# Kernel tuning notes

Measured on AMD Instinct MI355X. Metric: run time of the kernel, lower is better.

Reference implementation:

```python
import jax, jax.numpy as jnp
import numpy as np

B, KOBJ, NS, NK = 32, 100, 16, 8
EMB, FEAT, HID, OUT, COMB = 1024, 2052, 1024, 3000, 512


def _pseudo_coord(bb_centre):
    # bb_centre (B,K,2) -> polar pseudo coords (B,K,K,2) = (rho, theta)
    d = bb_centre[:, :, None, :] - bb_centre[:, None, :, :]
    rho = jnp.sqrt(d[..., 0] ** 2 + d[..., 1] ** 2)
    theta = jnp.arctan2(d[..., 0], d[..., 1])
    return jnp.stack([rho, theta], axis=-1)


def _gauss_weights(pseudo, mr, mt, pr, pt):
    # pseudo (B,K,NS,2); kernel params (NK,) -> weights (B,K,NS,NK)
    rho = pseudo[..., 0:1]
    theta = pseudo[..., 1:2]
    w_rho = jnp.exp(-0.5 * (rho - mr) ** 2 / (1e-14 + pr ** 2))
    fa = jnp.abs(theta - mt)
    sa = jnp.abs(2.0 * jnp.pi - fa)
    w_th = jnp.exp(-0.5 * jnp.minimum(fa, sa) ** 2 / (1e-14 + pt ** 2))
    w = w_rho * w_th
    w = jnp.where(jnp.isnan(w), 0.0, w)
    return w / jnp.sum(w, axis=-1, keepdims=True)  # normalise over kernels


def _graph_conv(feats, pseudo, conv_w, mr, mt, pr, pt):
    # feats (B,K,NS,F), conv_w (NK,F,out_k) -> (B,K,NK*out_k)
    w = _gauss_weights(pseudo, mr, mt, pr, pt)          # (B,K,NS,NK)
    agg = jnp.einsum('bksm,bksf->bkmf', w, feats)       # per-kernel neighbour sum
    out = jnp.einsum('bkmf,mfo->bkmo', agg, conv_w)     # per-kernel linear
    return out.reshape(out.shape[0], out.shape[1], -1)  # kernel-major concat


def _neighbourhood(feats, pseudo, adj, weight):
    # topk over adjacency rows; softmax over topk values (== the per-row loop softmax)
    top_v, top_i = jax.lax.top_k(adj, NS)               # (B,K,NS)
    a = jax.nn.softmax(top_v, axis=-1)
    nb_f = jax.vmap(lambda f, i: f[i])(feats, top_i)    # (B,K,NS,F)
    nb_p = jnp.take_along_axis(pseudo, top_i[..., None], axis=2)  # (B,K,NS,2)
    if weight:
        nb_f = a[..., None] * nb_f
    return nb_f, nb_p


def _forward(question, image, K, W_lproj, b_lproj, W_e1, b_e1, W_e2, b_e2,
             conv_w1, mean_rho1, mean_theta1, prec_rho1, prec_theta1,
             conv_w2, mean_rho2, mean_theta2, prec_rho2, prec_theta2,
             W_o1, b_o1, W_o2, b_o2):
    bb = image[:, :, -4:]
    bb_size = bb[:, :, 2:] - bb[:, :, :2]
    bb_centre = bb[:, :, :2] + 0.5 * bb_size
    pseudo = _pseudo_coord(bb_centre)                   # (B,K,K,2)

    qenc = question @ W_lproj + b_lproj                 # (B,HID)
    qrep = jnp.broadcast_to(qenc[:, None, :], (image.shape[0], K, qenc.shape[-1]))
    cat = jnp.concatenate([image, qrep], axis=-1)       # (B,K,FEAT+HID)

    # GraphLearner: two relu linears then gram matrix
    h = jax.nn.relu(cat @ W_e1 + b_e1)
    h = jax.nn.relu(h @ W_e2 + b_e2)                    # (B,K,COMB)
    adj = jnp.einsum('bkc,blc->bkl', h, h)              # (B,K,K)

    nb_f, nb_p = _neighbourhood(image, pseudo, adj, weight=True)
    g1 = jax.nn.relu(_graph_conv(nb_f, nb_p, conv_w1, mean_rho1, mean_theta1, prec_rho1, prec_theta1))
    nb_f2, nb_p2 = _neighbourhood(g1, pseudo, adj, weight=False)
    g2 = jax.nn.relu(_graph_conv(nb_f2, nb_p2, conv_w2, mean_rho2, mean_theta2, prec_rho2, prec_theta2))
    g2 = jnp.max(g2, axis=1)                            # (B,HID)

    hh = jax.nn.relu(qenc) * g2
    h1 = jax.nn.relu(hh @ W_o1 + b_o1)
    logits = h1 @ W_o2 + b_o2
    return logits, adj


def setup_inputs() -> dict:
    key = jax.random.key(0)
    ks = jax.random.split(key, 17)
    s = jnp.float32(0.02)
    f32 = jnp.float32
    inp = {
        'question': jax.random.normal(ks[0], (B, EMB), f32),
        'image': jax.random.uniform(ks[1], (B, KOBJ, FEAT), f32),
        'K': KOBJ,
        'W_lproj': jax.random.normal(ks[2], (EMB, HID), f32) * s,
        'b_lproj': jnp.zeros((HID,), f32),
        'W_e1': jax.random.normal(ks[3], (FEAT + HID, COMB), f32) * s,
        'b_e1': jnp.zeros((COMB,), f32),
        'W_e2': jax.random.normal(ks[4], (COMB, COMB), f32) * s,
        'b_e2': jnp.zeros((COMB,), f32),
        'conv_w1': jax.random.normal(ks[5], (NK, FEAT, 2 * HID // NK), f32) * s,
        'mean_rho1': jax.random.uniform(ks[6], (NK,), f32),
        'mean_theta1': jax.random.uniform(ks[7], (NK,), f32, -np.pi, np.pi),
        'prec_rho1': jax.random.uniform(ks[8], (NK,), f32),
        'prec_theta1': jax.random.uniform(ks[9], (NK,), f32),
        'conv_w2': jax.random.normal(ks[10], (NK, 2 * HID, HID // NK), f32) * s,
        'mean_rho2': jax.random.uniform(ks[11], (NK,), f32),
        'mean_theta2': jax.random.uniform(ks[12], (NK,), f32, -np.pi, np.pi),
        'prec_rho2': jax.random.uniform(ks[13], (NK,), f32),
        'prec_theta2': jax.random.uniform(ks[14], (NK,), f32),
        'W_o1': jax.random.normal(ks[15], (HID, OUT), f32) * s,
        'b_o1': jnp.zeros((OUT,), f32),
        'W_o2': jax.random.normal(ks[16], (OUT, OUT), f32) * s,
        'b_o2': jnp.zeros((OUT,), f32),
    }
    return inp


def reference(question, image, K, W_lproj, b_lproj, W_e1, b_e1, W_e2, b_e2,
              conv_w1, mean_rho1, mean_theta1, prec_rho1, prec_theta1,
              conv_w2, mean_rho2, mean_theta2, prec_rho2, prec_theta2,
              W_o1, b_o1, W_o2, b_o2):
    return _forward(question, image, K, W_lproj, b_lproj, W_e1, b_e1, W_e2, b_e2,
                    conv_w1, mean_rho1, mean_theta1, prec_rho1, prec_theta1,
                    conv_w2, mean_rho2, mean_theta2, prec_rho2, prec_theta2,
                    W_o1, b_o1, W_o2, b_o2)
```

## Files before the change

### kernel.cpp

```cpp
#include <hip/hip_runtime.h>
#include <math.h>
#include <stdint.h>

#define B_    32
#define KOBJ  100
#define NS_   16
#define NK_   8
#define EMB_  1024
#define FEAT_ 2052
#define HID_  1024
#define OUT_  3000
#define COMB_ 512

#define KP1   2112
#define KP2   2048
#define NO_P  3072
#define KO2   3008

typedef __attribute__((ext_vector_type(8))) short s16x8;
typedef __attribute__((ext_vector_type(4))) float f32x4;

__device__ inline short f2bf(float f) {
  uint32_t u = __builtin_bit_cast(uint32_t, f);
  u = (u + 0x7fff + ((u >> 16) & 1)) >> 16;
  return (short)u;
}
__device__ inline float bf2f(short s) {
  uint32_t u = ((uint32_t)(uint16_t)s) << 16;
  return __builtin_bit_cast(float, u);
}
__device__ inline void gload_lds16(const void* g, void* l) {
  __builtin_amdgcn_global_load_lds(
      (const __attribute__((address_space(1))) void*)g,
      (__attribute__((address_space(3))) void*)l, 16, 0, 0);
}
__device__ inline int xcd_remap(int fid, int nwg) {
  int q = nwg >> 3, r = nwg & 7;
  int x = fid & 7, l = fid >> 3;
  return (x < r ? x * (q + 1) : r * (q + 1) + (x - r) * q) + l;
}

#define IMG_CHUNKS (B_ * KOBJ * (KP1 / 8))
#define IMG_BLKS   ((IMG_CHUNKS + 255) / 256)
#define Q_CHUNKS   (B_ * (EMB_ / 8))
#define Q_BLKS     ((Q_CHUNKS + 255) / 256)
#define C_BLKS     ((B_ * KOBJ + 255) / 256)

__device__ inline void cvt8_split(const float* __restrict__ in, short* __restrict__ oh,
                                  short* __restrict__ ol, int K, int Kp, int idx) {
  int row = idx / (Kp / 8), c8 = (idx % (Kp / 8)) * 8;
  float f[8];
  if (c8 + 8 <= K) {
    const float* src = in + (size_t)row * K + c8;
    float4 a = *(const float4*)src;
    float4 b = *(const float4*)(src + 4);
    f[0] = a.x; f[1] = a.y; f[2] = a.z; f[3] = a.w;
    f[4] = b.x; f[5] = b.y; f[6] = b.z; f[7] = b.w;
  } else {
#pragma unroll
    for (int i = 0; i < 8; ++i) {
      int k = c8 + i;
      f[i] = (k < K) ? in[(size_t)row * K + k] : 0.f;
    }
  }
  s16x8 vh, vl;
#pragma unroll
  for (int i = 0; i < 8; ++i) {
    short h = f2bf(f[i]);
    vh[i] = h;
    vl[i] = f2bf(f[i] - bf2f(h));
  }
  *(s16x8*)(oh + (size_t)row * Kp + c8) = vh;
  *(s16x8*)(ol + (size_t)row * Kp + c8) = vl;
}

__global__ __launch_bounds__(256) void prep_inputs(
    const float* __restrict__ image, const float* __restrict__ question,
    short* __restrict__ imgb, short* __restrict__ imgl,
    short* __restrict__ qh, short* __restrict__ ql, float* __restrict__ cent) {
  int bb = blockIdx.x, tid = threadIdx.x;
  if (bb < IMG_BLKS) {
    int idx = bb * 256 + tid;
    if (idx < IMG_CHUNKS) cvt8_split(image, imgb, imgl, FEAT_, KP1, idx);
  } else if (bb < IMG_BLKS + Q_BLKS) {
    int idx = (bb - IMG_BLKS) * 256 + tid;
    if (idx < Q_CHUNKS) cvt8_split(question, qh, ql, EMB_, EMB_, idx);
  } else {
    int i = (bb - IMG_BLKS - Q_BLKS) * 256 + tid;
    if (i < B_ * KOBJ) {
      const float* bbx = image + (size_t)i * FEAT_ + (FEAT_ - 4);
      cent[i * 2 + 0] = 0.5f * (bbx[0] + bbx[2]);
      cent[i * 2 + 1] = 0.5f * (bbx[1] + bbx[3]);
    }
  }
}

struct TD {
  const float* in; short* oh; short* ol;
  int K, N, Kp, OPM, nkt, split, conv, cum;
};
struct TDs { TD d[8]; };

__global__ __launch_bounds__(256) void transpose_all(TDs ds) {
  __shared__ float s[64][65];
  int bid = blockIdx.x;
  int i = 0;
  while (i < 7 && bid >= ds.d[i].cum) ++i;
  const TD& d = ds.d[i];
  int local = bid - (i ? ds.d[i - 1].cum : 0);
  int k0 = (local % d.nkt) * 64, n0 = (local / d.nkt) * 64;
  int t = threadIdx.x;
  int rr = t >> 4, c4 = (t & 15) * 4;
  bool fullN = d.conv || (n0 + 64 <= d.N);
#pragma unroll
  for (int p = 0; p < 4; ++p) {
    int row = p * 16 + rr;
    int kg = k0 + row;
    float v0 = 0.f, v1 = 0.f, v2 = 0.f, v3 = 0.f;
    if (kg < d.K) {
      const float* src = d.conv
          ? d.in + ((size_t)(n0 / d.OPM) * d.K + kg) * d.OPM + (n0 % d.OPM) + c4
          : d.in + (size_t)kg * d.N + n0 + c4;
      if (fullN) {
        float4 v = *(const float4*)src;
        v0 = v.x; v1 = v.y; v2 = v.z; v3 = v.w;
      } else {
        int nb = n0 + c4;
        if (nb + 0 < d.N) v0 = src[0];
        if (nb + 1 < d.N) v1 = src[1];
        if (nb + 2 < d.N) v2 = src[2];
        if (nb + 3 < d.N) v3 = src[3];
      }
    }
    s[row][c4 + 0] = v0; s[row][c4 + 1] = v1;
    s[row][c4 + 2] = v2; s[row][c4 + 3] = v3;
  }
  __syncthreads();
  int nl = t >> 2, kc = (t & 3) << 4;
#pragma unroll
  for (int half = 0; half < 2; ++half) {
    s16x8 vh, vl;
#pragma unroll
    for (int j = 0; j < 8; ++j) {
      float f = s[kc + half * 8 + j][nl];
      short h = f2bf(f);
      vh[j] = h;
      vl[j] = f2bf(f - bf2f(h));
    }
    size_t o = (size_t)(n0 + nl) * d.Kp + k0 + kc + half * 8;
    *(s16x8*)(d.oh + o) = vh;
    if (d.split) *(s16x8*)(d.ol + o) = vl;
  }
}

template <int BM, int BN, int WR, int WC, bool SPLIT, bool RELU, bool BIAS, int OMODE,
          bool SPLITK, bool PB16>
__device__ __forceinline__ void gemm_body(
    char* smem, int bx, int by, int bz,
    const short* __restrict__ Ah, const short* __restrict__ Al,
    const short* __restrict__ Bh, const short* __restrict__ Bl,
    const float* __restrict__ bias,
    float* __restrict__ Cf, short* __restrict__ Ch, short* __restrict__ Cl,
    float* __restrict__ part, short* __restrict__ partb, int KS,
    int M, int N, int Kp, int ldc, int Nw) {
  constexpr int NWV = WR * WC;
  constexpr int WM = BM / WR, WN = BN / WC;
  constexpr int FM = WM / 16, FN = WN / 16;
  constexpr int ACH = BM / 8, BCH = BN / 8;
  constexpr int NCH = (ACH + BCH) * (SPLIT ? 2 : 1);
  char* AshC = smem;
  char* BshC = smem + BM * 128;
  char* AslC = smem + (BM + BN) * 128;
  char* BslC = smem + (2 * BM + BN) * 128;
  int tid = threadIdx.x, wave = tid >> 6, lane = tid & 63;
  int wr = wave / WC, wc = wave % WC;
  int r16 = lane & 15, kq = lane >> 4;
  int m0 = by * BM, n0 = bx * BN;
  int kb = SPLITK ? bz * KS : 0;
  int ke = SPLITK ? (kb + KS < Kp ? kb + KS : Kp) : Kp;
  f32x4 acc[FM][FN] = {};

  for (int k0 = kb; k0 < ke; k0 += 64) {
    __syncthreads();
    for (int c = wave; c < NCH; c += NWV) {
      int cc = c;
      const short* g;
      char* l;
      bool isA;
      if (cc < ACH) { isA = true; g = Ah; l = AshC; }
      else if (SPLIT && cc < 2 * ACH) { cc -= ACH; isA = true; g = Al; l = AslC; }
      else {
        cc -= SPLIT ? 2 * ACH : ACH;
        if (cc < BCH) { isA = false; g = Bh; l = BshC; }
        else { cc -= BCH; isA = false; g = Bl; l = BslC; }
      }
      int Lb = cc * 1024 + lane * 16;
      int row = Lb >> 7;
      int off = (Lb & 127) ^ ((row & 7) << 4);
      const short* gsrc = g + (size_t)((isA ? m0 : n0) + row) * Kp + k0 + (off >> 1);
      gload_lds16(gsrc, l + cc * 1024);
    }
    __syncthreads();
#pragma unroll
    for (int kk = 0; kk < 2; ++kk) {
      int woff = kk * 64 + kq * 16;
      s16x8 ah[FM], al[FM], bh[FN], bl[FN];
#pragma unroll
      for (int f = 0; f < FM; ++f) {
        int row = wr * WM + f * 16 + r16;
        int o = woff ^ ((row & 7) << 4);
        ah[f] = *(const s16x8*)(AshC + row * 128 + o);
        if (SPLIT) al[f] = *(const s16x8*)(AslC + row * 128 + o);
      }
#pragma unroll
      for (int gg = 0; gg < FN; ++gg) {
        int row = wc * WN + gg * 16 + r16;
        int o = woff ^ ((row & 7) << 4);
        bh[gg] = *(const s16x8*)(BshC + row * 128 + o);
        if (SPLIT) bl[gg] = *(const s16x8*)(BslC + row * 128 + o);
      }
#pragma unroll
      for (int f = 0; f < FM; ++f)
#pragma unroll
        for (int gg = 0; gg < FN; ++gg) {
          acc[f][gg] = __builtin_amdgcn_mfma_f32_16x16x32_bf16(ah[f], bh[gg], acc[f][gg], 0, 0, 0);
          if (SPLIT) {
            acc[f][gg] = __builtin_amdgcn_mfma_f32_16x16x32_bf16(ah[f], bl[gg], acc[f][gg], 0, 0, 0);
            acc[f][gg] = __builtin_amdgcn_mfma_f32_16x16x32_bf16(al[f], bh[gg], acc[f][gg], 0, 0, 0);
          }
        }
    }
  }
#pragma unroll
  for (int f = 0; f < FM; ++f)
#pragma unroll
    for (int gg = 0; gg < FN; ++gg)
#pragma unroll
      for (int r = 0; r < 4; ++r) {
        int m = m0 + wr * WM + f * 16 + (lane >> 4) * 4 + r;
        int n = n0 + wc * WN + gg * 16 + r16;
        if (m >= M || n >= Nw) continue;
        float v = (n < N) ? acc[f][gg][r] : 0.f;
        size_t idx = (size_t)m * ldc + n;
        if (SPLITK) {
          size_t pidx = (size_t)bz * M * ldc + idx;
          if (PB16) partb[pidx] = f2bf(v);
          else      part[pidx] = v;
        } else {
          if (BIAS && n < N) v += bias[n];
          if (RELU) v = fmaxf(v, 0.f);
          if (OMODE == 0) Cf[idx] = v;
          else if (OMODE == 1) {
            short h = f2bf(v);
            Ch[idx] = h;
            Cl[idx] = f2bf(v - bf2f(h));
          } else if (OMODE == 2) {
            Ch[idx] = f2bf(v);
          } else {
            Cf[idx] = v;
            short h = f2bf(v);
            Ch[idx] = h;
            Cl[idx] = f2bf(v - bf2f(h));
          }
        }
      }
}

template <int BM, int BN, int WR, int WC, bool SPLIT, bool RELU, bool BIAS, int OMODE,
          bool SPLITK, bool PB16>
__global__ __launch_bounds__(WR * WC * 64) void gemm_mx(
    const short* __restrict__ Ah, const short* __restrict__ Al,
    const short* __restrict__ Bh, const short* __restrict__ Bl,
    const float* __restrict__ bias,
    float* __restrict__ Cf, short* __restrict__ Ch, short* __restrict__ Cl,
    float* __restrict__ part, short* __restrict__ partb, int KS,
    int M, int N, int Kp, int ldc, int Nw) {
  __shared__ char smem_s[(BM + BN) * 128 * (SPLIT ? 2 : 1)];
  int gx = gridDim.x, gy = gridDim.y, gz = gridDim.z;
  int fid = (blockIdx.z * gy + blockIdx.y) * gx + blockIdx.x;
  int wg = xcd_remap(fid, gx * gy * gz);
  int bx = wg % gx, byz = wg / gx;
  int by = byz % gy, bz = byz / gy;
  gemm_body<BM, BN, WR, WC, SPLIT, RELU, BIAS, OMODE, SPLITK, PB16>(
      smem_s, bx, by, bz, Ah, Al, Bh, Bl, bias, Cf, Ch, Cl, part, partb, KS,
      M, N, Kp, ldc, Nw);
}

#define E1B 800
#define P1B 800
__global__ __launch_bounds__(512) void fused_e1_proj1(
    const short* __restrict__ imgb, const short* __restrict__ imgl,
    const short* __restrict__ we1ah, const short* __restrict__ we1al,
    float* __restrict__ partE,
    const short* __restrict__ cw1t, short* __restrict__ partP) {
  extern __shared__ char smem[];
  int fid = blockIdx.x;
  if (fid < E1B) {
    int wg = xcd_remap(fid, E1B);
    int gx = COMB_ / 64;
    int bx = wg % gx, t = wg / gx;
    int by = t % (B_ * KOBJ / 128), bz = t / (B_ * KOBJ / 128);
    gemm_body<128, 64, 4, 2, true, false, false, 0, true, false>(
        smem, bx, by, bz, imgb, imgl, we1ah, we1al, nullptr,
        nullptr, nullptr, nullptr, partE, nullptr, 576,
        B_ * KOBJ, COMB_, KP1, COMB_, COMB_);
  } else {
    int wg = xcd_remap(fid - E1B, P1B);
    int gx = 2 * HID_ / 128;
    int bx = wg % gx, t = wg / gx;
    int by = t % (B_ * KOBJ / 128), bz = t / (B_ * KOBJ / 128);
    gemm_body<128, 128, 2, 4, false, false, false, 0, true, true>(
        smem, bx, by, bz, imgb, nullptr, cw1t, nullptr, nullptr,
        nullptr, nullptr, nullptr, nullptr, partP, 1056,
        B_ * KOBJ, 2 * HID_, KP1, 2 * HID_, 2 * HID_);
  }
}

template <int OMODE, bool RELU, bool BIAS, bool BCAST, bool PB16>
__global__ void reduce_split(const float* __restrict__ part, const short* __restrict__ partb,
                             int SK, size_t pstride,
                             const float* __restrict__ bias, const float* __restrict__ bcast,
                             int bcols, float* __restrict__ Cf, short* __restrict__ Ch,
                             short* __restrict__ Cl, int M, int N, int ldIn, int ldOut) {
  int idx4 = blockIdx.x * 256 + threadIdx.x;
  int ld4 = ldIn >> 2;
  if (idx4 >= M * ld4) return;
  int m = idx4 / ld4;
  int n = (idx4 - m * ld4) << 2;
  size_t base = (size_t)m * ldIn + n;
  float a[4] = {0.f, 0.f, 0.f, 0.f};
  for (int s = 0; s < SK; ++s) {
    if (PB16) {
      short4 p = *(const short4*)(partb + (size_t)s * pstride + base);
      const short* pp = (const short*)&p;
#pragma unroll
      for (int j = 0; j < 4; ++j) a[j] += bf2f(pp[j]);
    } else {
      float4 p = *(const float4*)(part + (size_t)s * pstride + base);
      a[0] += p.x; a[1] += p.y; a[2] += p.z; a[3] += p.w;
    }
  }
#pragma unroll
  for (int j = 0; j < 4; ++j) {
    int nn = n + j;
    if (nn < N) {
      if (BCAST) a[j] += bcast[(size_t)(m / KOBJ) * bcols + nn];
      if (BIAS) a[j] += bias[nn];
    }
    if (RELU) a[j] = fmaxf(a[j], 0.f);
  }
  if (n >= ldOut) return;
  size_t o = (size_t)m * ldOut + n;
  if (OMODE == 0) {
    *(float4*)(Cf + o) = make_float4(a[0], a[1], a[2], a[3]);
  } else if (OMODE == 1) {
    short4 hh, ll;
    short* hp = (short*)&hh; short* lp = (short*)&ll;
#pragma unroll
    for (int j = 0; j < 4; ++j) {
      short h = f2bf(a[j]);
      hp[j] = h;
      lp[j] = f2bf(a[j] - bf2f(h));
    }
    *(short4*)(Ch + o) = hh;
    *(short4*)(Cl + o) = ll;
  } else {
    short4 hh;
    short* hp = (short*)&hh;
#pragma unroll
    for (int j = 0; j < 4; ++j) hp[j] = f2bf(a[j]);
    *(short4*)(Ch + o) = hh;
  }
}

__global__ __launch_bounds__(512) void adj_mfma(const short* __restrict__ Hh,
                                                const short* __restrict__ Hl,
                                                float* __restrict__ adj) {
  __shared__ short Ash[128 * 64];
  __shared__ short Asl[128 * 64];
  int tid = threadIdx.x, wave = tid >> 6, lane = tid & 63;
  int wr = wave >> 2, wc = wave & 3;
  int r16 = lane & 15, kq = lane >> 4;
  int b = blockIdx.x;
  const short* baseh = Hh + (size_t)b * KOBJ * COMB_;
  const short* basel = Hl + (size_t)b * KOBJ * COMB_;
  f32x4 acc[4][2] = {};
  for (int k0 = 0; k0 < COMB_; k0 += 64) {
    __syncthreads();
    for (int c = wave; c < 32; c += 8) {
      int cc = c & 15;
      bool hi = c < 16;
      int Lb = cc * 1024 + lane * 16;
      int row = Lb >> 7;
      int off = (Lb & 127) ^ ((row & 7) << 4);
      const short* gsrc = (hi ? baseh : basel) + (size_t)row * COMB_ + k0 + (off >> 1);
      gload_lds16(gsrc, (char*)(hi ? Ash : Asl) + cc * 1024);
    }
    __syncthreads();
#pragma unroll
    for (int kk = 0; kk < 2; ++kk) {
      int woff = kk * 64 + kq * 16;
      s16x8 ah[4], al[4], bh[2], bl[2];
#pragma unroll
      for (int f = 0; f < 4; ++f) {
        int row = wr * 64 + f * 16 + r16;
        int o = woff ^ ((row & 7) << 4);
        ah[f] = *(const s16x8*)((const char*)Ash + row * 128 + o);
        al[f] = *(const s16x8*)((const char*)Asl + row * 128 + o);
      }
#pragma unroll
      for (int g = 0; g < 2; ++g) {
        int row = wc * 32 + g * 16 + r16;
        int o = woff ^ ((row & 7) << 4);
        bh[g] = *(const s16x8*)((const char*)Ash + row * 128 + o);
        bl[g] = *(const s16x8*)((const char*)Asl + row * 128 + o);
      }
#pragma unroll
      for (int f = 0; f < 4; ++f)
#pragma unroll
        for (int g = 0; g < 2; ++g) {
          acc[f][g] = __builtin_amdgcn_mfma_f32_16x16x32_bf16(ah[f], bh[g], acc[f][g], 0, 0, 0);
          acc[f][g] = __builtin_amdgcn_mfma_f32_16x16x32_bf16(ah[f], bl[g], acc[f][g], 0, 0, 0);
          acc[f][g] = __builtin_amdgcn_mfma_f32_16x16x32_bf16(al[f], bh[g], acc[f][g], 0, 0, 0);
        }
    }
  }
#pragma unroll
  for (int f = 0; f < 4; ++f)
#pragma unroll
    for (int g = 0; g < 2; ++g)
#pragma unroll
      for (int r = 0; r < 4; ++r) {
        int m = wr * 64 + f * 16 + (lane >> 4) * 4 + r;
        int n = wc * 32 + g * 16 + r16;
        if (m < KOBJ && n < KOBJ)
          adj[((size_t)b * KOBJ + m) * KOBJ + n] = acc[f][g][r];
      }
}

__global__ __launch_bounds__(256) void topk_weights_kernel(
    const float* __restrict__ adj, const float* __restrict__ cent,
    const float* __restrict__ mr1, const float* __restrict__ mt1,
    const float* __restrict__ pr1, const float* __restrict__ pt1,
    const float* __restrict__ mr2, const float* __restrict__ mt2,
    const float* __restrict__ pr2, const float* __restrict__ pt2,
    int* __restrict__ topi, float* __restrict__ c1, float* __restrict__ c2) {
  int row = blockIdx.x * 4 + (threadIdx.x >> 6);
  int lane = threadIdx.x & 63;
  int b = row / KOBJ, k = row % KOBJ;
  const float* ar = adj + (size_t)row * KOBJ;
  float v0 = (lane < KOBJ) ? ar[lane] : -INFINITY;
  float v1 = (lane + 64 < KOBJ) ? ar[lane + 64] : -INFINITY;
  int i0 = lane, i1 = lane + 64;
  float tv[NS_];
  int ti[NS_];
#pragma unroll
  for (int s = 0; s < NS_; ++s) {
    bool p0 = (v0 > v1) || (v0 == v1 && i0 < i1);
    float bv = p0 ? v0 : v1;
    int bi = p0 ? i0 : i1;
#pragma unroll
    for (int off = 32; off > 0; off >>= 1) {
      float ov = __shfl_xor(bv, off);
      int oi = __shfl_xor(bi, off);
      if (ov > bv || (ov == bv && oi < bi)) { bv = ov; bi = oi; }
    }
    tv[s] = bv; ti[s] = bi;
    if (bi == i0) v0 = -INFINITY;
    if (bi == i1) v1 = -INFINITY;
  }
  float mx = tv[0], sum = 0.f, av[NS_];
#pragma unroll
  for (int s = 0; s < NS_; ++s) { av[s] = expf(tv[s] - mx); sum += av[s]; }
  if (lane < NS_) {
    int j = ti[lane];
    topi[(size_t)row * NS_ + lane] = j;
    float cx = cent[(b * KOBJ + k) * 2 + 0], cy = cent[(b * KOBJ + k) * 2 + 1];
    float dx = cx - cent[(b * KOBJ + j) * 2 + 0];
    float dy = cy - cent[(b * KOBJ + j) * 2 + 1];
    float rho = sqrtf(dx * dx + dy * dy);
    float th = atan2f(dx, dy);
    float w1[NK_], w2[NK_], s1 = 0.f, s2 = 0.f;
#pragma unroll
    for (int m = 0; m < NK_; ++m) {
      {
        float pr = pr1[m], pt = pt1[m], dr = rho - mr1[m];
        float wr = expf(-0.5f * dr * dr / (1e-14f + pr * pr));
        float fa = fabsf(th - mt1[m]);
        float sa = fabsf(6.283185307179586f - fa);
        float da = fminf(fa, sa);
        float wt = expf(-0.5f * da * da / (1e-14f + pt * pt));
        float w = wr * wt;
        if (w != w) w = 0.f;
        w1[m] = w; s1 += w;
      }
      {
        float pr = pr2[m], pt = pt2[m], dr = rho - mr2[m];
        float wr = expf(-0.5f * dr * dr / (1e-14f + pr * pr));
        float fa = fabsf(th - mt2[m]);
        float sa = fabsf(6.283185307179586f - fa);
        float da = fminf(fa, sa);
        float wt = expf(-0.5f * da * da / (1e-14f + pt * pt));
        float w = wr * wt;
        if (w != w) w = 0.f;
        w2[m] = w; s2 += w;
      }
    }
    float as = av[lane] / sum;
#pragma unroll
    for (int m = 0; m < NK_; ++m) {
      c1[((size_t)row * NS_ + lane) * NK_ + m] = as * (w1[m] / s1);
      c2[((size_t)row * NS_ + lane) * NK_ + m] = w2[m] / s2;
    }
  }
}

template <int VEC, bool BF16OUT>
__global__ __launch_bounds__(256) void combine_kernel(
    const short* __restrict__ proj, const float* __restrict__ coeff,
    const int* __restrict__ topi, float* __restrict__ outf, short* __restrict__ outb,
    int N, int mshift) {
  int row = xcd_remap(blockIdx.x, gridDim.x);
  int b = row / KOBJ;
  __shared__ int ids[NS_];
  __shared__ float cs[NS_ * NK_];
  int tid = threadIdx.x;
  if (tid < NS_) ids[tid] = topi[(size_t)row * NS_ + tid];
  else if (tid >= 32 && tid < 32 + NS_ * NK_) cs[tid - 32] = coeff[(size_t)row * NS_ * NK_ + (tid - 32)];
  __syncthreads();
  int n = tid * VEC;
  if (n >= N) return;
  int m = n >> mshift;
  float acc[VEC];
#pragma unroll
  for (int j = 0; j < VEC; ++j) acc[j] = 0.f;
#pragma unroll
  for (int s = 0; s < NS_; ++s) {
    float cc = cs[s * NK_ + m];
    const short* p = proj + ((size_t)b * KOBJ + ids[s]) * N + n;
    if (VEC == 8) {
      s16x8 v = *(const s16x8*)p;
#pragma unroll
      for (int j = 0; j < 8; ++j) acc[j] = fmaf(cc, bf2f(v[j]), acc[j]);
    } else {
      short4 v = *(const short4*)p;
      const short* vp = (const short*)&v;
#pragma unroll
      for (int j = 0; j < 4; ++j) acc[j] = fmaf(cc, bf2f(vp[j]), acc[j]);
    }
  }
#pragma unroll
  for (int j = 0; j < VEC; ++j) acc[j] = fmaxf(acc[j], 0.f);
  if (BF16OUT) {
    if (VEC == 8) {
      s16x8 o;
#pragma unroll
      for (int j = 0; j < 8; ++j) o[j] = f2bf(acc[j]);
      *(s16x8*)(outb + (size_t)row * N + n) = o;
    } else {
      short4 o;
      short* op = (short*)&o;
#pragma unroll
      for (int j = 0; j < 4; ++j) op[j] = f2bf(acc[j]);
      *(short4*)(outb + (size_t)row * N + n) = o;
    }
  } else {
    if (VEC == 4) {
      *(float4*)(outf + (size_t)row * N + n) = make_float4(acc[0], acc[1], acc[2], acc[3]);
    } else {
#pragma unroll
      for (int j = 0; j < VEC; ++j) outf[(size_t)row * N + n + j] = acc[j];
    }
  }
}

__global__ void reduce_hh_kernel(const float* __restrict__ g2, const float* __restrict__ qenc,
                                 short* __restrict__ hhb) {
  int i = blockIdx.x * blockDim.x + threadIdx.x;
  if (i >= B_ * HID_) return;
  int b = i >> 10, n = i & (HID_ - 1);
  const float* p = g2 + (size_t)b * KOBJ * HID_ + n;
  float mx = -INFINITY;
  for (int k = 0; k < KOBJ; ++k) mx = fmaxf(mx, p[(size_t)k * HID_]);
  hhb[i] = f2bf(fmaxf(qenc[i], 0.f) * mx);
}

extern "C" void kernel_launch(void* const* d_in, const int* in_sizes, int n_in,
                              void* d_out, int out_size, void* d_ws, size_t ws_size,
                              hipStream_t stream) {
  const float* question = (const float*)d_in[0];
  const float* image    = (const float*)d_in[1];
  const float* W_lproj  = (const float*)d_in[3];
  const float* b_lproj  = (const float*)d_in[4];
  const float* W_e1     = (const float*)d_in[5];
  const float* b_e1     = (const float*)d_in[6];
  const float* W_e2     = (const float*)d_in[7];
  const float* b_e2     = (const float*)d_in[8];
  const float* conv_w1  = (const float*)d_in[9];
  const float* mr1 = (const float*)d_in[10];
  const float* mt1 = (const float*)d_in[11];
  const float* pr1 = (const float*)d_in[12];
  const float* pt1 = (const float*)d_in[13];
  const float* conv_w2  = (const float*)d_in[14];
  const float* mr2 = (const float*)d_in[15];
  const float* mt2 = (const float*)d_in[16];
  const float* pr2 = (const float*)d_in[17];
  const float* pt2 = (const float*)d_in[18];
  const float* W_o1 = (const float*)d_in[19];
  const float* b_o1 = (const float*)d_in[20];
  const float* W_o2 = (const float*)d_in[21];
  const float* b_o2 = (const float*)d_in[22];

  float* out = (float*)d_out;
  float* logits = out;
  float* adj = out + B_ * OUT_;

  char* ws = (char*)d_ws;
  size_t off = 0;
  auto alloc = [&](size_t bytes) { char* p = ws + off; off += (bytes + 255) & ~((size_t)255); return p; };
  float* qenc  = (float*)alloc((size_t)B_ * HID_ * 4);
  short* qh    = (short*)alloc((size_t)B_ * EMB_ * 2);
  short* ql    = (short*)alloc((size_t)B_ * EMB_ * 2);
  short* qeh   = (short*)alloc((size_t)B_ * HID_ * 2);
  short* qel   = (short*)alloc((size_t)B_ * HID_ * 2);
  short* wlph  = (short*)alloc((size_t)EMB_ * HID_ * 2);
  short* wlpl  = (short*)alloc((size_t)EMB_ * HID_ * 2);
  short* we1ah = (short*)alloc((size_t)COMB_ * KP1 * 2);
  short* we1al = (short*)alloc((size_t)COMB_ * KP1 * 2);
  short* we1bh = (short*)alloc((size_t)COMB_ * HID_ * 2);
  short* we1bl = (short*)alloc((size_t)COMB_ * HID_ * 2);
  short* we2h  = (short*)alloc((size_t)COMB_ * COMB_ * 2);
  short* we2l  = (short*)alloc((size_t)COMB_ * COMB_ * 2);
  float* q1    = (float*)alloc((size_t)B_ * COMB_ * 4);
  short* h1h   = (short*)alloc((size_t)B_ * KOBJ * COMB_ * 2);
  short* h1l   = (short*)alloc((size_t)B_ * KOBJ * COMB_ * 2);
  short* h2h   = (short*)alloc((size_t)(B_ * KOBJ + 128) * COMB_ * 2);
  short* h2l   = (short*)alloc((size_t)(B_ * KOBJ + 128) * COMB_ * 2);
  float* cent  = (float*)alloc((size_t)B_ * KOBJ * 2 * 4);
  int*   topi  = (int*)alloc((size_t)B_ * KOBJ * NS_ * 4);
  float* c1    = (float*)alloc((size_t)B_ * KOBJ * NS_ * NK_ * 4);
  float* c2    = (float*)alloc((size_t)B_ * KOBJ * NS_ * NK_ * 4);
  short* imgb  = (short*)alloc((size_t)B_ * KOBJ * KP1 * 2);
  short* imgl  = (short*)alloc((size_t)B_ * KOBJ * KP1 * 2);
  short* cw1t  = (short*)alloc((size_t)(2 * HID_) * KP1 * 2);
  short* cw2t  = (short*)alloc((size_t)HID_ * KP2 * 2);
  short* proj1b = (short*)alloc((size_t)B_ * KOBJ * 2 * HID_ * 2);
  short* g1b   = (short*)alloc((size_t)B_ * KOBJ * KP2 * 2);
  short* proj2b = (short*)alloc((size_t)B_ * KOBJ * HID_ * 2);
  float* g2    = (float*)alloc((size_t)B_ * KOBJ * HID_ * 4);
  short* hhb   = (short*)alloc((size_t)B_ * HID_ * 2);
  short* wo1t  = (short*)alloc((size_t)NO_P * HID_ * 2);
  short* wo2t  = (short*)alloc((size_t)NO_P * KO2 * 2);
  short* h1ob  = (short*)alloc((size_t)B_ * KO2 * 2);
  float* partE = (float*)alloc((size_t)4 * B_ * KOBJ * COMB_ * 4);
  short* partP = (short*)alloc((size_t)2 * B_ * KOBJ * 2 * HID_ * 2);
  (void)ws_size; (void)in_sizes; (void)n_in; (void)out_size;

  dim3 blk(256), blk512(512);

  prep_inputs<<<dim3(IMG_BLKS + Q_BLKS + C_BLKS), blk, 0, stream>>>(
      image, question, imgb, imgl, qh, ql, cent);

  {
    TDs ds;
    int cum = 0;
    auto set = [&](int i, const float* in, short* oh, short* ol, int K, int N, int Kp,
                   int OPM, int nnt, int split, int conv) {
      int nkt = Kp / 64;
      cum += nkt * nnt;
      ds.d[i] = TD{in, oh, ol, K, N, Kp, OPM, nkt, split, conv, cum};
    };
    set(0, W_lproj, wlph, wlpl, EMB_, HID_, EMB_, 0, HID_ / 64, 1, 0);
    set(1, W_e1, we1ah, we1al, FEAT_, COMB_, KP1, 0, COMB_ / 64, 1, 0);
    set(2, W_e1 + (size_t)FEAT_ * COMB_, we1bh, we1bl, HID_, COMB_, HID_, 0, COMB_ / 64, 1, 0);
    set(3, W_e2, we2h, we2l, COMB_, COMB_, COMB_, 0, COMB_ / 64, 1, 0);
    set(4, conv_w1, cw1t, nullptr, FEAT_, 2 * HID_, KP1, 2 * HID_ / NK_, 2 * HID_ / 64, 0, 1);
    set(5, conv_w2, cw2t, nullptr, 2 * HID_, HID_, KP2, HID_ / NK_, HID_ / 64, 0, 1);
    set(6, W_o1, wo1t, nullptr, HID_, OUT_, HID_, 0, NO_P / 64, 0, 0);
    set(7, W_o2, wo2t, nullptr, OUT_, OUT_, KO2, 0, NO_P / 64, 0, 0);
    transpose_all<<<dim3(cum), blk, 0, stream>>>(ds);
  }

  gemm_mx<32, 64, 2, 2, true, false, true, 3, false, false><<<dim3(HID_ / 64, 1, 1), blk, 0, stream>>>(
      qh, ql, wlph, wlpl, b_lproj, qenc, qeh, qel, nullptr, nullptr, 0, B_, HID_, EMB_, HID_, HID_);
  gemm_mx<32, 64, 2, 2, true, false, false, 0, false, false><<<dim3(COMB_ / 64, 1, 1), blk, 0, stream>>>(
      qeh, qel, we1bh, we1bl, nullptr, q1, nullptr, nullptr, nullptr, nullptr, 0, B_, COMB_, HID_, COMB_, COMB_);
  fused_e1_proj1<<<dim3(E1B + P1B), blk512, 49152, stream>>>(
      imgb, imgl, we1ah, we1al, partE, cw1t, partP);
  reduce_split<1, true, true, true, false><<<dim3(B_ * KOBJ * COMB_ / 4 / 256), blk, 0, stream>>>(
      partE, nullptr, 4, (size_t)B_ * KOBJ * COMB_, b_e1, q1, COMB_, nullptr, h1h, h1l,
      B_ * KOBJ, COMB_, COMB_, COMB_);
  gemm_mx<128, 64, 4, 2, true, false, false, 0, true, false><<<dim3(COMB_ / 64, B_ * KOBJ / 128, 4), blk512, 0, stream>>>(
      h1h, h1l, we2h, we2l, nullptr, nullptr, nullptr, nullptr, partE, nullptr, 128,
      B_ * KOBJ, COMB_, COMB_, COMB_, COMB_);
  reduce_split<1, true, true, false, false><<<dim3(B_ * KOBJ * COMB_ / 4 / 256), blk, 0, stream>>>(
      partE, nullptr, 4, (size_t)B_ * KOBJ * COMB_, b_e2, nullptr, 0, nullptr, h2h, h2l,
      B_ * KOBJ, COMB_, COMB_, COMB_);
  adj_mfma<<<dim3(B_), blk512, 0, stream>>>(h2h, h2l, adj);
  topk_weights_kernel<<<dim3(B_ * KOBJ / 4), blk, 0, stream>>>(
      adj, cent, mr1, mt1, pr1, pt1, mr2, mt2, pr2, pt2, topi, c1, c2);
  reduce_split<2, false, false, false, true><<<dim3(B_ * KOBJ * 2 * HID_ / 4 / 256), blk, 0, stream>>>(
      nullptr, partP, 2, (size_t)B_ * KOBJ * 2 * HID_, nullptr, nullptr, 0, nullptr, proj1b, nullptr,
      B_ * KOBJ, 2 * HID_, 2 * HID_, 2 * HID_);
  combine_kernel<8, true><<<dim3(B_ * KOBJ), blk, 0, stream>>>(
      proj1b, c1, topi, nullptr, g1b, 2 * HID_, 8);
  gemm_mx<128, 128, 2, 4, false, false, false, 0, true, true><<<dim3(HID_ / 128, B_ * KOBJ / 128, 4), blk512, 0, stream>>>(
      g1b, nullptr, cw2t, nullptr, nullptr, nullptr, nullptr, nullptr, nullptr, partP, 512,
      B_ * KOBJ, HID_, KP2, HID_, HID_);
  reduce_split<2, false, false, false, true><<<dim3(B_ * KOBJ * HID_ / 4 / 256), blk, 0, stream>>>(
      nullptr, partP, 4, (size_t)B_ * KOBJ * HID_, nullptr, nullptr, 0, nullptr, proj2b, nullptr,
      B_ * KOBJ, HID_, HID_, HID_);
  combine_kernel<4, false><<<dim3(B_ * KOBJ), blk, 0, stream>>>(
      proj2b, c2, topi, g2, nullptr, HID_, 7);
  reduce_hh_kernel<<<dim3((B_ * HID_ + 255) / 256), blk, 0, stream>>>(g2, qenc, hhb);
  gemm_mx<32, 128, 1, 4, false, false, false, 0, true, false><<<dim3(NO_P / 128, 1, 16), blk, 0, stream>>>(
      hhb, nullptr, wo1t, nullptr, nullptr, nullptr, nullptr, nullptr, partE, nullptr, 64,
      B_, OUT_, HID_, KO2, KO2);
  reduce_split<2, true, true, false, false><<<dim3((B_ * KO2 / 4 + 255) / 256), blk, 0, stream>>>(
      partE, nullptr, 16, (size_t)B_ * KO2, b_o1, nullptr, 0, nullptr, h1ob, nullptr,
      B_, OUT_, KO2, KO2);
  gemm_mx<32, 128, 1, 4, false, false, false, 0, true, false><<<dim3(NO_P / 128, 1, 16), blk, 0, stream>>>(
      h1ob, nullptr, wo2t, nullptr, nullptr, nullptr, nullptr, nullptr, partE, nullptr, 192,
      B_, OUT_, KO2, KO2, KO2);
  reduce_split<0, false, true, false, false><<<dim3((B_ * KO2 / 4 + 255) / 256), blk, 0, stream>>>(
      partE, nullptr, 16, (size_t)B_ * KO2, b_o2, nullptr, 0, logits, nullptr, nullptr,
      B_, OUT_, KO2, OUT_);
}
```

Before: 338.8 us.

## Drop split-K for proj1 GEMM and merge input prep into transpose launch

The proj1 GEMM inside the fused e1/proj1 kernel no longer uses split-K. It now writes bf16 output straight to proj1b, which removes a reduce_split launch and the round trip of bf16 partial sums through memory. The separate prep_inputs kernel is folded into the weight transpose launch as extra blocks, saving one launch. The trade-off is fewer proj1 workgroups (400 instead of 800), each doing the full K loop. That may lengthen the tail of the fused kernel, though the e1 blocks still provide parallelism.

```diff
diff --git a/kernel.cpp b/kernel.cpp
--- a/kernel.cpp
+++ b/kernel.cpp
@@ -74,42 +74,42 @@
   *(s16x8*)(ol + (size_t)row * Kp + c8) = vl;
 }
 
-__global__ __launch_bounds__(256) void prep_inputs(
-    const float* __restrict__ image, const float* __restrict__ question,
-    short* __restrict__ imgb, short* __restrict__ imgl,
-    short* __restrict__ qh, short* __restrict__ ql, float* __restrict__ cent) {
-  int bb = blockIdx.x, tid = threadIdx.x;
-  if (bb < IMG_BLKS) {
-    int idx = bb * 256 + tid;
-    if (idx < IMG_CHUNKS) cvt8_split(image, imgb, imgl, FEAT_, KP1, idx);
-  } else if (bb < IMG_BLKS + Q_BLKS) {
-    int idx = (bb - IMG_BLKS) * 256 + tid;
-    if (idx < Q_CHUNKS) cvt8_split(question, qh, ql, EMB_, EMB_, idx);
-  } else {
-    int i = (bb - IMG_BLKS - Q_BLKS) * 256 + tid;
-    if (i < B_ * KOBJ) {
-      const float* bbx = image + (size_t)i * FEAT_ + (FEAT_ - 4);
-      cent[i * 2 + 0] = 0.5f * (bbx[0] + bbx[2]);
-      cent[i * 2 + 1] = 0.5f * (bbx[1] + bbx[3]);
-    }
-  }
-}
-
 struct TD {
   const float* in; short* oh; short* ol;
   int K, N, Kp, OPM, nkt, split, conv, cum;
 };
 struct TDs { TD d[8]; };
 
-__global__ __launch_bounds__(256) void transpose_all(TDs ds) {
+__global__ __launch_bounds__(256) void prep_all(
+    TDs ds, int tcum,
+    const float* __restrict__ image, const float* __restrict__ question,
+    short* __restrict__ imgb, short* __restrict__ imgl,
+    short* __restrict__ qh, short* __restrict__ ql, float* __restrict__ cent) {
+  int bid = blockIdx.x, t = threadIdx.x;
+  if (bid >= tcum) {
+    int bb = bid - tcum;
+    if (bb < IMG_BLKS) {
+      int idx = bb * 256 + t;
+      if (idx < IMG_CHUNKS) cvt8_split(image, imgb, imgl, FEAT_, KP1, idx);
+    } else if (bb < IMG_BLKS + Q_BLKS) {
+      int idx = (bb - IMG_BLKS) * 256 + t;
+      if (idx < Q_CHUNKS) cvt8_split(question, qh, ql, EMB_, EMB_, idx);
+    } else {
+      int i = (bb - IMG_BLKS - Q_BLKS) * 256 + t;
+      if (i < B_ * KOBJ) {
+        const float* bbx = image + (size_t)i * FEAT_ + (FEAT_ - 4);
+        cent[i * 2 + 0] = 0.5f * (bbx[0] + bbx[2]);
+        cent[i * 2 + 1] = 0.5f * (bbx[1] + bbx[3]);
+      }
+    }
+    return;
+  }
   __shared__ float s[64][65];
-  int bid = blockIdx.x;
   int i = 0;
   while (i < 7 && bid >= ds.d[i].cum) ++i;
   const TD& d = ds.d[i];
   int local = bid - (i ? ds.d[i - 1].cum : 0);
   int k0 = (local % d.nkt) * 64, n0 = (local / d.nkt) * 64;
-  int t = threadIdx.x;
   int rr = t >> 4, c4 = (t & 15) * 4;
   bool fullN = d.conv || (n0 + 64 <= d.N);
 #pragma unroll
@@ -287,12 +287,12 @@
 }
 
 #define E1B 800
-#define P1B 800
+#define P1B 400
 __global__ __launch_bounds__(512) void fused_e1_proj1(
     const short* __restrict__ imgb, const short* __restrict__ imgl,
     const short* __restrict__ we1ah, const short* __restrict__ we1al,
     float* __restrict__ partE,
-    const short* __restrict__ cw1t, short* __restrict__ partP) {
+    const short* __restrict__ cw1t, short* __restrict__ proj1b) {
   extern __shared__ char smem[];
   int fid = blockIdx.x;
   if (fid < E1B) {
@@ -307,11 +307,10 @@
   } else {
     int wg = xcd_remap(fid - E1B, P1B);
     int gx = 2 * HID_ / 128;
-    int bx = wg % gx, t = wg / gx;
-    int by = t % (B_ * KOBJ / 128), bz = t / (B_ * KOBJ / 128);
-    gemm_body<128, 128, 2, 4, false, false, false, 0, true, true>(
-        smem, bx, by, bz, imgb, nullptr, cw1t, nullptr, nullptr,
-        nullptr, nullptr, nullptr, nullptr, partP, 1056,
+    int bx = wg % gx, by = wg / gx;
+    gemm_body<128, 128, 2, 4, false, false, false, 2, false, false>(
+        smem, bx, by, 0, imgb, nullptr, cw1t, nullptr, nullptr,
+        nullptr, proj1b, nullptr, nullptr, nullptr, 0,
         B_ * KOBJ, 2 * HID_, KP1, 2 * HID_, 2 * HID_);
   }
 }
@@ -653,13 +652,10 @@
   short* wo2t  = (short*)alloc((size_t)NO_P * KO2 * 2);
   short* h1ob  = (short*)alloc((size_t)B_ * KO2 * 2);
   float* partE = (float*)alloc((size_t)4 * B_ * KOBJ * COMB_ * 4);
-  short* partP = (short*)alloc((size_t)2 * B_ * KOBJ * 2 * HID_ * 2);
+  short* partP = (short*)alloc((size_t)4 * B_ * KOBJ * HID_ * 2);
   (void)ws_size; (void)in_sizes; (void)n_in; (void)out_size;
 
   dim3 blk(256), blk512(512);
-
-  prep_inputs<<<dim3(IMG_BLKS + Q_BLKS + C_BLKS), blk, 0, stream>>>(
-      image, question, imgb, imgl, qh, ql, cent);
 
   {
     TDs ds;
@@ -678,7 +674,8 @@
     set(5, conv_w2, cw2t, nullptr, 2 * HID_, HID_, KP2, HID_ / NK_, HID_ / 64, 0, 1);
     set(6, W_o1, wo1t, nullptr, HID_, OUT_, HID_, 0, NO_P / 64, 0, 0);
     set(7, W_o2, wo2t, nullptr, OUT_, OUT_, KO2, 0, NO_P / 64, 0, 0);
-    transpose_all<<<dim3(cum), blk, 0, stream>>>(ds);
+    prep_all<<<dim3(cum + IMG_BLKS + Q_BLKS + C_BLKS), blk, 0, stream>>>(
+        ds, cum, image, question, imgb, imgl, qh, ql, cent);
   }
 
   gemm_mx<32, 64, 2, 2, true, false, true, 3, false, false><<<dim3(HID_ / 64, 1, 1), blk, 0, stream>>>(
@@ -686,7 +683,7 @@
   gemm_mx<32, 64, 2, 2, true, false, false, 0, false, false><<<dim3(COMB_ / 64, 1, 1), blk, 0, stream>>>(
       qeh, qel, we1bh, we1bl, nullptr, q1, nullptr, nullptr, nullptr, nullptr, 0, B_, COMB_, HID_, COMB_, COMB_);
   fused_e1_proj1<<<dim3(E1B + P1B), blk512, 49152, stream>>>(
-      imgb, imgl, we1ah, we1al, partE, cw1t, partP);
+      imgb, imgl, we1ah, we1al, partE, cw1t, proj1b);
   reduce_split<1, true, true, true, false><<<dim3(B_ * KOBJ * COMB_ / 4 / 256), blk, 0, stream>>>(
       partE, nullptr, 4, (size_t)B_ * KOBJ * COMB_, b_e1, q1, COMB_, nullptr, h1h, h1l,
       B_ * KOBJ, COMB_, COMB_, COMB_);
@@ -699,9 +696,6 @@
   adj_mfma<<<dim3(B_), blk512, 0, stream>>>(h2h, h2l, adj);
   topk_weights_kernel<<<dim3(B_ * KOBJ / 4), blk, 0, stream>>>(
       adj, cent, mr1, mt1, pr1, pt1, mr2, mt2, pr2, pt2, topi, c1, c2);
-  reduce_split<2, false, false, false, true><<<dim3(B_ * KOBJ * 2 * HID_ / 4 / 256), blk, 0, stream>>>(
-      nullptr, partP, 2, (size_t)B_ * KOBJ * 2 * HID_, nullptr, nullptr, 0, nullptr, proj1b, nullptr,
-      B_ * KOBJ, 2 * HID_, 2 * HID_, 2 * HID_);
   combine_kernel<8, true><<<dim3(B_ * KOBJ), blk, 0, stream>>>(
       proj1b, c1, topi, nullptr, g1b, 2 * HID_, 8);
   gemm_mx<128, 128, 2, 4, false, false, false, 0, true, true><<<dim3(HID_ / 128, B_ * KOBJ / 128, 4), blk512, 0, stream>>>(
```

Result: faster. 318.7 us (-5.9%).
